# Kernel optimization log

Measured on AMD Instinct MI355X. Metric: run time of the kernel, lower is better.

The kernel has to match this reference:

```python
import jax, jax.numpy as jnp
import numpy as np

NUM_HEADS = 8
BLOCK_SIZE = 32   # tokens per block
WINDOW = 64       # window radius in blocks -> attends to blocks [i-64, i+64]


def setup_inputs() -> dict:
    key = jax.random.key(0)
    ks = jax.random.split(key, 5)
    B, N, C = 8, 8192, 512
    s = 0.02
    return {
        "x": jax.random.normal(ks[0], (B, N, C), dtype=jnp.float32),
        # torch Linear(dim, 3*dim): y = x @ W.T + b; we store W already transposed [in, out]
        "W_qkv": jax.random.normal(ks[1], (C, 3 * C), dtype=jnp.float32) * s,
        "b_qkv": jax.random.normal(ks[2], (3 * C,), dtype=jnp.float32) * s,
        "W_proj": jax.random.normal(ks[3], (C, C), dtype=jnp.float32) * s,
        "b_proj": jax.random.normal(ks[4], (C,), dtype=jnp.float32) * s,
    }


def reference(x, W_qkv, b_qkv, W_proj, b_proj):
    B, N, C = x.shape
    h = NUM_HEADS
    dh = C // h
    scale = jnp.asarray(dh, x.dtype) ** -0.5

    # qkv projection, then the module's head-interleaved split:
    # rearrange 'b n (h d) -> b h n d' with d = 3C/h, chunk(3) on last dim,
    # rearrange back 'b h n d -> b n (h d)'. Equivalent to:
    qkv = (x @ W_qkv + b_qkv).reshape(B, N, h, 3 * dh)
    q = qkv[..., :dh].reshape(B, N, C)
    k = qkv[..., dh:2 * dh].reshape(B, N, C)
    v = qkv[..., 2 * dh:].reshape(B, N, C)

    # dynamic blocking (N chosen divisible by BLOCK_SIZE -> no padding)
    nb = N // BLOCK_SIZE
    qb = q.reshape(B, nb, BLOCK_SIZE, C)
    kb = k.reshape(B, nb, BLOCK_SIZE, C)
    vb = v.reshape(B, nb, BLOCK_SIZE, C)

    # per-offset block attention: query block i, position s attends to
    # position s of every block j in [i-WINDOW, i+WINDOW]
    attn = jnp.einsum('bisc,bjsc->bisj', qb, kb) * scale  # [B, nb, s, nb]
    i_idx = jnp.arange(nb)[:, None]
    j_idx = jnp.arange(nb)[None, :]
    band = (j_idx >= i_idx - WINDOW) & (j_idx <= i_idx + WINDOW)  # [nb, nb]
    neg = jnp.finfo(attn.dtype).min
    attn = jnp.where(band[None, :, None, :], attn, neg)
    attn = jax.nn.softmax(attn, axis=-1)
    out = jnp.einsum('bisj,bjsc->bisc', attn, vb)  # [B, nb, s, C]
    out = out.reshape(B, N, C)

    # 'b n (h d) -> b n h d -> b n (h d)' is the identity
    return out @ W_proj + b_proj
```

## Files before the change

### kernel.cpp

```cpp
#include <hip/hip_runtime.h>
#include <hip/hip_bf16.h>
#include <stdint.h>

#define B_   8
#define N_   8192
#define C_   512
#define NB   256
#define WIN  64

typedef __attribute__((ext_vector_type(8))) short short8;
typedef __attribute__((ext_vector_type(4))) float f32x4;
typedef __hip_bfloat16 bf16;

__device__ __forceinline__ void gload_lds16(const void* g, void* l) {
  __builtin_amdgcn_global_load_lds((const __attribute__((address_space(1))) void*)g,
                                   (__attribute__((address_space(3))) void*)l, 16, 0, 0);
}

__device__ __forceinline__ f32x4 mfma16(short8 a, short8 b, f32x4 c) {
  return __builtin_amdgcn_mfma_f32_16x16x32_bf16(a, b, c, 0, 0, 0);
}


__global__ __launch_bounds__(256) void k_conv_x(const float4* __restrict__ x,
                                                ushort4* __restrict__ xb) {
  size_t idx = (size_t)blockIdx.x * 256 + threadIdx.x;
  float4 v = x[idx];
  union { ushort4 u; bf16 b[4]; } o;
  o.b[0] = __float2bfloat16(v.x); o.b[1] = __float2bfloat16(v.y);
  o.b[2] = __float2bfloat16(v.z); o.b[3] = __float2bfloat16(v.w);
  xb[idx] = o.u;
}

__global__ __launch_bounds__(256) void k_conv_wqkv(const float* __restrict__ W,
                                                   const float* __restrict__ bq,
                                                   bf16* __restrict__ Wt,
                                                   float* __restrict__ bperm) {
  int o = blockIdx.x;
  int part = o >> 9;
  int c = o & 511;
  int h = c >> 6, d = c & 63;
  int src = h * 192 + part * 64 + d;
  for (int kk = threadIdx.x; kk < 512; kk += 256)
    Wt[(size_t)o * 512 + kk] = __float2bfloat16(W[(size_t)kk * 1536 + src]);
  if (threadIdx.x == 0) bperm[o] = bq[src];
}

__global__ __launch_bounds__(256) void k_conv_wproj(const float* __restrict__ W,
                                                    bf16* __restrict__ Wt) {
  int o = blockIdx.x;
  for (int kk = threadIdx.x; kk < 512; kk += 256)
    Wt[(size_t)o * 512 + kk] = __float2bfloat16(W[(size_t)kk * 512 + o]);
}

template <int EPI>
__global__ __launch_bounds__(512, 2) void k_gemm(const bf16* __restrict__ A,
                                                 const bf16* __restrict__ Bt,
                                                 const float* __restrict__ bias,
                                                 bf16* __restrict__ qb,
                                                 bf16* __restrict__ kb,
                                                 bf16* __restrict__ vb,
                                                 float* __restrict__ outf,
                                                 int NT) {
  extern __shared__ bf16 sm[];
  const int tid = threadIdx.x;
  const int lane = tid & 63, wid = tid >> 6;
  const int wr = wid >> 2, wcn = wid & 3;
  const int l15 = lane & 15, l4 = lane >> 4;

  const int nwg = gridDim.x;
  const int cpx = nwg >> 3;
  const int swz = (blockIdx.x & 7) * cpx + (blockIdx.x >> 3);
  const int mt = swz / NT, nt = swz % NT;
  const size_t m0 = (size_t)mt * 256;
  const int n0 = nt * 256;

  f32x4 acc[8][4];
#pragma unroll
  for (int fi = 0; fi < 8; ++fi)
#pragma unroll
    for (int fj = 0; fj < 4; ++fj) acc[fi][fj] = (f32x4){0.f, 0.f, 0.f, 0.f};

#define STAGEG(slot, k0)                                                       \
  {                                                                            \
    bf16* Adst = sm + (slot) * 32768;                                          \
    bf16* Bdst = Adst + 16384;                                                 \
    _Pragma("unroll") for (int i = 0; i < 4; ++i) {                            \
      int li = i * 512 + tid;                                                  \
      int row = li >> 3, ch = li & 7;                                          \
      int chs = ch ^ (row & 7);                                                \
      gload_lds16(A + (m0 + row) * 512 + (k0) + chs * 8,                       \
                  (char*)Adst + li * 16);                                      \
      gload_lds16(Bt + (size_t)(n0 + row) * 512 + (k0) + chs * 8,              \
                  (char*)Bdst + li * 16);                                      \
    }                                                                          \
  }

  STAGEG(0, 0);
  for (int t = 0; t < 8; ++t) {
    if (t < 7) {
      STAGEG((t + 1) & 1, (t + 1) * 64);
      asm volatile("s_waitcnt vmcnt(8)" ::: "memory");
    } else {
      asm volatile("s_waitcnt vmcnt(0)" ::: "memory");
    }
    __builtin_amdgcn_s_barrier();
    __builtin_amdgcn_sched_barrier(0);
    const bf16* Ap = sm + (t & 1) * 32768;
    const bf16* Bp = Ap + 16384;
#pragma unroll
    for (int ks = 0; ks < 2; ++ks) {
      short8 a[8], b[4];
#pragma unroll
      for (int fi = 0; fi < 8; ++fi) {
        int ra = wr * 128 + fi * 16 + l15;
        a[fi] = *(const short8*)&Ap[ra * 64 + (((ks * 4 + l4) ^ (ra & 7)) << 3)];
      }
#pragma unroll
      for (int fj = 0; fj < 4; ++fj) {
        int rb = wcn * 64 + fj * 16 + l15;
        b[fj] = *(const short8*)&Bp[rb * 64 + (((ks * 4 + l4) ^ (rb & 7)) << 3)];
      }
      __builtin_amdgcn_s_setprio(1);
#pragma unroll
      for (int fi = 0; fi < 8; ++fi)
#pragma unroll
        for (int fj = 0; fj < 4; ++fj)
          acc[fi][fj] = mfma16(a[fi], b[fj], acc[fi][fj]);
      __builtin_amdgcn_s_setprio(0);
    }
    __builtin_amdgcn_sched_barrier(0);
    __builtin_amdgcn_s_barrier();
  }
#undef STAGEG

  if (EPI == 0) {
#pragma unroll
    for (int fi = 0; fi < 8; ++fi)
#pragma unroll
      for (int fj = 0; fj < 4; ++fj) {
        int o = n0 + wcn * 64 + fj * 16 + l15;
        float bia = bias[o];
        int part = o >> 9;
        int c = o & 511;
        bf16* dst = part == 0 ? qb : (part == 1 ? kb : vb);
#pragma unroll
        for (int r = 0; r < 4; ++r) {
          size_t m = m0 + wr * 128 + fi * 16 + l4 * 4 + r;
          int bidx = (int)(m >> 13);
          int n = (int)(m & 8191);
          int blk = n >> 5, s = n & 31;
          size_t di = (((size_t)(bidx * 32 + s) * 256 + blk) << 9) | c;
          dst[di] = __float2bfloat16(acc[fi][fj][r] + bia);
        }
      }
  } else {
#pragma unroll
    for (int fi = 0; fi < 8; ++fi)
#pragma unroll
      for (int fj = 0; fj < 4; ++fj) {
        int o = n0 + wcn * 64 + fj * 16 + l15;
        float bia = bias[o];
#pragma unroll
        for (int r = 0; r < 4; ++r) {
          size_t m = m0 + wr * 128 + fi * 16 + l4 * 4 + r;
          outf[m * 512 + o] = acc[fi][fj][r] + bia;
        }
      }
  }
}

__global__ __launch_bounds__(256) void k_transpose_v(const bf16* __restrict__ v,
                                                     bf16* __restrict__ vT) {
  __shared__ bf16 t[32][36];
  int bs = blockIdx.x, j0 = blockIdx.y * 32, c0 = blockIdx.z * 32;
  const bf16* src = v + (size_t)bs * NB * C_;
  bf16* dst = vT + (size_t)bs * C_ * NB;
  int r = threadIdx.x >> 3, c4 = (threadIdx.x & 7) * 4;
  *(ushort4*)&t[r][c4] = *(const ushort4*)(src + (size_t)(j0 + r) * C_ + c0 + c4);
  __syncthreads();
  union { ushort4 u; bf16 b[4]; } o;
  o.b[0] = t[c4 + 0][r]; o.b[1] = t[c4 + 1][r];
  o.b[2] = t[c4 + 2][r]; o.b[3] = t[c4 + 3][r];
  *(ushort4*)(dst + (size_t)(c0 + r) * NB + j0 + c4) = o.u;
}

#define QS_OFF   0
#define KB_OFF   32768
#define VB_OFF   98304
#define SS_OFF   131072
#define PS_OFF   135296
#define SR_OFF   137856
#define MR_OFF   141952
#define LR_OFF   142080
#define AL_OFF   142208
#define ATTN_LDS 142336

__global__ __launch_bounds__(512) void k_attn(const bf16* __restrict__ qg,
                                              const bf16* __restrict__ kg,
                                              const bf16* __restrict__ vTg,
                                              bf16* __restrict__ outb) {
  extern __shared__ char smc[];
  float* Ssf  = (float*)(smc + SS_OFF);
  bf16*  Psb  = (bf16*)(smc + PS_OFF);
  float* Sred = (float*)(smc + SR_OFF);
  float* mrow = (float*)(smc + MR_OFF);
  float* lrow = (float*)(smc + LR_OFF);
  float* alph = (float*)(smc + AL_OFF);

  const int tid = threadIdx.x, lane = tid & 63, wid = tid >> 6;
  const int l15 = lane & 15, l4 = lane >> 4;
  const int gt = (blockIdx.x & 7) * 256 + (blockIdx.x >> 3);
  const int bs = gt >> 3;
  const int b = bs >> 5, s = bs & 31;
  const int i0 = (gt & 7) * 32;
  const int jlo = max(0, i0 - WIN);
  const int jhi = min(NB - 1, i0 + 31 + WIN);
  const int nch = (jhi - jlo + 1) >> 5;
  const bf16* Qb = qg + (size_t)bs * NB * C_;
  const bf16* Kb = kg + (size_t)bs * NB * C_;
  const bf16* Vb = vTg + (size_t)bs * C_ * NB;

  const int qh_qk = (wid >> 2) & 1, jh = (wid >> 1) & 1, ks = wid & 1;
  const int qh_pv = wid >> 2, cq = wid & 3;

  f32x4 O[8];
#pragma unroll
  for (int f = 0; f < 8; ++f) O[f] = (f32x4){0.f, 0.f, 0.f, 0.f};

  if (tid < 32) { mrow[tid] = -1e30f; lrow[tid] = 0.f; }

#pragma unroll
  for (int q = 0; q < 4; ++q) {
    int li = q * 512 + tid;
    int row = li >> 6, g = (li & 63) ^ (row & 15);
    gload_lds16(Qb + (size_t)(i0 + row) * C_ + g * 8, smc + QS_OFF + li * 16);
  }
#pragma unroll
  for (int q = 0; q < 4; ++q) {
    int li = q * 512 + tid;
    int row = li >> 6, g = (li & 63) ^ (row & 15);
    gload_lds16(Kb + (size_t)(jlo + row) * C_ + g * 8, smc + KB_OFF + li * 16);
  }

  for (int t = 0; t < nch; ++t) {
    const int j0 = jlo + t * 32;
    asm volatile("s_waitcnt vmcnt(0) lgkmcnt(0)" ::: "memory");
    __builtin_amdgcn_s_barrier();
    __builtin_amdgcn_sched_barrier(0);

#pragma unroll
    for (int q = 0; q < 4; ++q) {
      int li = q * 512 + tid;
      int c = li >> 2, g = (li & 3) ^ (c & 3);
      gload_lds16(Vb + (size_t)c * NB + j0 + g * 8, smc + VB_OFF + li * 16);
    }
    if (t + 1 < nch) {
      int jn = j0 + 32;
      char* kdst = smc + KB_OFF + ((t + 1) & 1) * 32768;
#pragma unroll
      for (int q = 0; q < 4; ++q) {
        int li = q * 512 + tid;
        int row = li >> 6, g = (li & 63) ^ (row & 15);
        gload_lds16(Kb + (size_t)(jn + row) * C_ + g * 8, kdst + li * 16);
      }
    }

    {
      const int arow = qh_qk * 16 + l15;
      const int brow = jh * 16 + l15;
      const char* Qbase = smc + QS_OFF + arow * 1024;
      const char* Kbase = smc + KB_OFF + (t & 1) * 32768 + brow * 1024;
      f32x4 a0 = (f32x4){0.f, 0.f, 0.f, 0.f}, a1 = a0;
      __builtin_amdgcn_s_setprio(1);
#pragma unroll
      for (int cc = 0; cc < 8; ++cc) {
        int sa = (ks * 32 + cc * 4 + l4) ^ (arow & 15);
        int sb = (ks * 32 + cc * 4 + l4) ^ (brow & 15);
        short8 av = *(const short8*)(Qbase + sa * 16);
        short8 bv = *(const short8*)(Kbase + sb * 16);
        if (cc & 1) a1 = mfma16(av, bv, a1);
        else        a0 = mfma16(av, bv, a0);
      }
      __builtin_amdgcn_s_setprio(0);
      f32x4 acc = a0 + a1;
      if (ks) {
        *(f32x4*)&Sred[(wid >> 1) * 256 + lane * 4] = acc;
      }
      asm volatile("s_waitcnt lgkmcnt(0)" ::: "memory");
      __builtin_amdgcn_s_barrier();
      __builtin_amdgcn_sched_barrier(0);
      if (!ks) {
        f32x4 su = acc + *(f32x4*)&Sred[(wid >> 1) * 256 + lane * 4];
        int jg = j0 + jh * 16 + l15;
#pragma unroll
        for (int r = 0; r < 4; ++r) {
          int i_in = qh_qk * 16 + l4 * 4 + r;
          int i_abs = i0 + i_in;
          bool valid = (jg >= i_abs - WIN) && (jg <= i_abs + WIN);
          Ssf[i_in * 33 + jh * 16 + l15] = valid ? su[r] * 0.125f : -1e30f;
        }
      }
      asm volatile("s_waitcnt lgkmcnt(0)" ::: "memory");
      __builtin_amdgcn_s_barrier();
      __builtin_amdgcn_sched_barrier(0);
    }

    {
      int row = tid >> 4, u = tid & 15;
      float s0 = Ssf[row * 33 + u], s1 = Ssf[row * 33 + u + 16];
      float mc = fmaxf(s0, s1);
      mc = fmaxf(mc, __shfl_xor(mc, 1));
      mc = fmaxf(mc, __shfl_xor(mc, 2));
      mc = fmaxf(mc, __shfl_xor(mc, 4));
      mc = fmaxf(mc, __shfl_xor(mc, 8));
      float mo = mrow[row];
      float mn = fmaxf(mo, mc);
      float a = __expf(mo - mn);
      float p0 = __expf(s0 - mn), p1 = __expf(s1 - mn);
      float ps = p0 + p1;
      ps += __shfl_xor(ps, 1);
      ps += __shfl_xor(ps, 2);
      ps += __shfl_xor(ps, 4);
      ps += __shfl_xor(ps, 8);
      if (u == 0) {
        lrow[row] = lrow[row] * a + ps;
        mrow[row] = mn;
        alph[row] = a;
      }
      Psb[row * 40 + u] = __float2bfloat16(p0);
      Psb[row * 40 + u + 16] = __float2bfloat16(p1);
    }
    if (t + 1 < nch)
      asm volatile("s_waitcnt vmcnt(4) lgkmcnt(0)" ::: "memory");
    else
      asm volatile("s_waitcnt vmcnt(0) lgkmcnt(0)" ::: "memory");
    __builtin_amdgcn_s_barrier();
    __builtin_amdgcn_sched_barrier(0);

    {
      float ar[4];
#pragma unroll
      for (int r = 0; r < 4; ++r) ar[r] = alph[qh_pv * 16 + l4 * 4 + r];
      short8 pa = *(const short8*)(smc + PS_OFF + (qh_pv * 16 + l15) * 80 + l4 * 16);
      __builtin_amdgcn_s_setprio(1);
#pragma unroll
      for (int f = 0; f < 8; ++f) {
        int c = cq * 128 + f * 16 + l15;
        short8 vv = *(const short8*)(smc + VB_OFF + c * 64 + ((l4 ^ (c & 3)) << 4));
#pragma unroll
        for (int r = 0; r < 4; ++r) O[f][r] *= ar[r];
        O[f] = mfma16(pa, vv, O[f]);
      }
      __builtin_amdgcn_s_setprio(0);
    }
    __builtin_amdgcn_sched_barrier(0);
  }

  asm volatile("s_waitcnt lgkmcnt(0)" ::: "memory");
  __builtin_amdgcn_s_barrier();
  {
    float lr[4];
#pragma unroll
    for (int r = 0; r < 4; ++r) lr[r] = 1.f / lrow[qh_pv * 16 + l4 * 4 + r];
#pragma unroll
    for (int f = 0; f < 8; ++f) {
      int c = cq * 128 + f * 16 + l15;
#pragma unroll
      for (int r = 0; r < 4; ++r) {
        int il = qh_pv * 16 + l4 * 4 + r;
        int n = (i0 + il) * 32 + s;
        outb[((size_t)b * N_ + n) * C_ + c] = __float2bfloat16(O[f][r] * lr[r]);
      }
    }
  }
}

extern "C" void kernel_launch(void* const* d_in, const int* in_sizes, int n_in,
                              void* d_out, int out_size, void* d_ws, size_t ws_size,
                              hipStream_t stream) {
  const float* x = (const float*)d_in[0];
  const float* Wqkv = (const float*)d_in[1];
  const float* bqkv = (const float*)d_in[2];
  const float* Wproj = (const float*)d_in[3];
  const float* bproj = (const float*)d_in[4];

  char* ws = (char*)d_ws;
  const size_t SLOT = 67108864ull;
  bf16* slotA = (bf16*)ws;
  bf16* slotB = (bf16*)(ws + SLOT);
  bf16* Wqkv_t = (bf16*)(ws + 2 * SLOT);
  bf16* Wproj_t = (bf16*)(ws + 2 * SLOT + 1572864);
  float* bias_perm = (float*)(ws + 2 * SLOT + 1572864 + 524288);
  bf16* qbuf = (bf16*)d_out;
  bf16* kbuf = qbuf + 33554432ull;

  static int attr_done = 0;
  if (!attr_done) {
    hipFuncSetAttribute((const void*)k_gemm<0>,
                        hipFuncAttributeMaxDynamicSharedMemorySize, 131072);
    hipFuncSetAttribute((const void*)k_gemm<1>,
                        hipFuncAttributeMaxDynamicSharedMemorySize, 131072);
    hipFuncSetAttribute((const void*)k_attn,
                        hipFuncAttributeMaxDynamicSharedMemorySize, ATTN_LDS);
    attr_done = 1;
  }

  k_conv_x<<<32768, 256, 0, stream>>>((const float4*)x, (ushort4*)slotA);
  k_conv_wqkv<<<1536, 256, 0, stream>>>(Wqkv, bqkv, Wqkv_t, bias_perm);
  k_conv_wproj<<<512, 256, 0, stream>>>(Wproj, Wproj_t);

  k_gemm<0><<<256 * 6, 512, 131072, stream>>>(slotA, Wqkv_t, bias_perm,
                                              qbuf, kbuf, slotB, nullptr, 6);
  k_transpose_v<<<dim3(256, 8, 16), 256, 0, stream>>>(slotB, slotA);
  k_attn<<<2048, 512, ATTN_LDS, stream>>>(qbuf, kbuf, slotA, slotB);
  k_gemm<1><<<256 * 2, 512, 131072, stream>>>(slotB, Wproj_t, bproj,
                                              nullptr, nullptr, nullptr, (float*)d_out, 2);
}
```

Before: 339.1 us.

## Fuse V transpose into QKV GEMM epilogue, tile weight conversion, restructure GEMM loop

The QKV GEMM epilogue now writes V directly in transposed [bs, c, blk] layout, which removes the separate transpose kernel and its extra pass over V. Weight conversion kernels are merged into one LDS-tiled transpose kernel, so global reads are coalesced. The GEMM main loop changes its warp-to-fragment mapping (interleaved rows and columns), loads all fragments for a 64-wide K slice up front, and waits on vmcnt(0) at the end of each iteration instead of vmcnt(8). The transposed V stores are 2-byte scattered writes with a 512-byte stride, which may cost more than the removed transpose kernel did.

```diff
diff --git a/kernel.cpp b/kernel.cpp
--- a/kernel.cpp
+++ b/kernel.cpp
@@ -32,25 +32,30 @@
   xb[idx] = o.u;
 }
 
-__global__ __launch_bounds__(256) void k_conv_wqkv(const float* __restrict__ W,
-                                                   const float* __restrict__ bq,
-                                                   bf16* __restrict__ Wt,
-                                                   float* __restrict__ bperm) {
-  int o = blockIdx.x;
-  int part = o >> 9;
-  int c = o & 511;
-  int h = c >> 6, d = c & 63;
-  int src = h * 192 + part * 64 + d;
-  for (int kk = threadIdx.x; kk < 512; kk += 256)
-    Wt[(size_t)o * 512 + kk] = __float2bfloat16(W[(size_t)kk * 1536 + src]);
-  if (threadIdx.x == 0) bperm[o] = bq[src];
-}
-
-__global__ __launch_bounds__(256) void k_conv_wproj(const float* __restrict__ W,
-                                                    bf16* __restrict__ Wt) {
-  int o = blockIdx.x;
-  for (int kk = threadIdx.x; kk < 512; kk += 256)
-    Wt[(size_t)o * 512 + kk] = __float2bfloat16(W[(size_t)kk * 512 + o]);
+__global__ __launch_bounds__(256) void k_conv_w(const float* __restrict__ W,
+                                                const float* __restrict__ bsrc,
+                                                bf16* __restrict__ Wt,
+                                                float* __restrict__ bperm,
+                                                int ldw, int qkv) {
+  __shared__ float tile[32][65];
+  const int cc = blockIdx.x, k0 = blockIdx.y * 32;
+  const int src0 = cc * 64;
+  const int o0 = qkv ? ((cc % 3) * 512 + (cc / 3) * 64) : src0;
+  const int tid = threadIdx.x;
+#pragma unroll
+  for (int q = 0; q < 8; ++q) {
+    int li = q * 256 + tid;
+    int r = li >> 6, c = li & 63;
+    tile[r][c] = W[(size_t)(k0 + r) * ldw + src0 + c];
+  }
+  __syncthreads();
+#pragma unroll
+  for (int q = 0; q < 8; ++q) {
+    int li = q * 256 + tid;
+    int c2 = li >> 5, kk = li & 31;
+    Wt[(size_t)(o0 + c2) * 512 + k0 + kk] = __float2bfloat16(tile[kk][c2]);
+  }
+  if (qkv && blockIdx.y == 0 && tid < 64) bperm[o0 + tid] = bsrc[src0 + tid];
 }
 
 template <int EPI>
@@ -62,7 +67,7 @@
                                                  bf16* __restrict__ vb,
                                                  float* __restrict__ outf,
                                                  int NT) {
-  extern __shared__ bf16 sm[];
+  extern __shared__ char gsm[];
   const int tid = threadIdx.x;
   const int lane = tid & 63, wid = tid >> 6;
   const int wr = wid >> 2, wcn = wid & 3;
@@ -81,77 +86,105 @@
 #pragma unroll
     for (int fj = 0; fj < 4; ++fj) acc[fi][fj] = (f32x4){0.f, 0.f, 0.f, 0.f};
 
-#define STAGEG(slot, k0)                                                       \
+#define STAGE(E, K0)                                                           \
   {                                                                            \
-    bf16* Adst = sm + (slot) * 32768;                                          \
-    bf16* Bdst = Adst + 16384;                                                 \
-    _Pragma("unroll") for (int i = 0; i < 4; ++i) {                            \
-      int li = i * 512 + tid;                                                  \
-      int row = li >> 3, ch = li & 7;                                          \
-      int chs = ch ^ (row & 7);                                                \
-      gload_lds16(A + (m0 + row) * 512 + (k0) + chs * 8,                       \
-                  (char*)Adst + li * 16);                                      \
-      gload_lds16(Bt + (size_t)(n0 + row) * 512 + (k0) + chs * 8,              \
-                  (char*)Bdst + li * 16);                                      \
+    _Pragma("unroll") for (int q = 0; q < 4; ++q) {                            \
+      int li = q * 512 + tid;                                                  \
+      int r = li >> 3, g = (li & 7) ^ (r & 7);                                 \
+      gload_lds16(A + (m0 + r) * 512 + (K0) + g * 8,                           \
+                  gsm + (E) * 65536 + li * 16);                                \
     }                                                                          \
-  }
-
-  STAGEG(0, 0);
+    _Pragma("unroll") for (int q = 0; q < 4; ++q) {                            \
+      int li = q * 512 + tid;                                                  \
+      int r = li >> 3, g = (li & 7) ^ (r & 7);                                 \
+      gload_lds16(Bt + (size_t)(n0 + r) * 512 + (K0) + g * 8,                  \
+                  gsm + (E) * 65536 + 32768 + li * 16);                        \
+    }                                                                          \
+  }
+
+  STAGE(0, 0);
+  asm volatile("s_waitcnt vmcnt(0)" ::: "memory");
+  __builtin_amdgcn_s_barrier();
+  __builtin_amdgcn_sched_barrier(0);
+
   for (int t = 0; t < 8; ++t) {
-    if (t < 7) {
-      STAGEG((t + 1) & 1, (t + 1) * 64);
-      asm volatile("s_waitcnt vmcnt(8)" ::: "memory");
-    } else {
-      asm volatile("s_waitcnt vmcnt(0)" ::: "memory");
-    }
+    const int d = t & 1;
+    if (t < 7) STAGE(d ^ 1, (t + 1) * 64);
+    __builtin_amdgcn_sched_barrier(0);
+    const char* Ab = gsm + d * 65536;
+    const char* Bb = Ab + 32768;
+
+    short8 a0[4][2], a1[4][2], bfr[4][2];
+#pragma unroll
+    for (int f = 0; f < 4; ++f) {
+      int ra = f * 32 + wr * 16 + l15;
+      const char* base = Ab + ra * 128;
+      a0[f][0] = *(const short8*)(base + ((l4 ^ (ra & 7)) << 4));
+      a0[f][1] = *(const short8*)(base + (((4 + l4) ^ (ra & 7)) << 4));
+    }
+#pragma unroll
+    for (int f = 0; f < 4; ++f) {
+      int rb = f * 64 + wcn * 16 + l15;
+      const char* base = Bb + rb * 128;
+      bfr[f][0] = *(const short8*)(base + ((l4 ^ (rb & 7)) << 4));
+      bfr[f][1] = *(const short8*)(base + (((4 + l4) ^ (rb & 7)) << 4));
+    }
+#pragma unroll
+    for (int f = 0; f < 4; ++f) {
+      int ra = 128 + f * 32 + wr * 16 + l15;
+      const char* base = Ab + ra * 128;
+      a1[f][0] = *(const short8*)(base + ((l4 ^ (ra & 7)) << 4));
+      a1[f][1] = *(const short8*)(base + (((4 + l4) ^ (ra & 7)) << 4));
+    }
+
+    __builtin_amdgcn_s_setprio(1);
+#pragma unroll
+    for (int f = 0; f < 4; ++f)
+#pragma unroll
+      for (int g = 0; g < 4; ++g) {
+        acc[f][g] = mfma16(a0[f][0], bfr[g][0], acc[f][g]);
+        acc[f][g] = mfma16(a0[f][1], bfr[g][1], acc[f][g]);
+      }
+#pragma unroll
+    for (int f = 0; f < 4; ++f)
+#pragma unroll
+      for (int g = 0; g < 4; ++g) {
+        acc[4 + f][g] = mfma16(a1[f][0], bfr[g][0], acc[4 + f][g]);
+        acc[4 + f][g] = mfma16(a1[f][1], bfr[g][1], acc[4 + f][g]);
+      }
+    __builtin_amdgcn_s_setprio(0);
+
+    __builtin_amdgcn_sched_barrier(0);
+    asm volatile("s_waitcnt vmcnt(0)" ::: "memory");
     __builtin_amdgcn_s_barrier();
     __builtin_amdgcn_sched_barrier(0);
-    const bf16* Ap = sm + (t & 1) * 32768;
-    const bf16* Bp = Ap + 16384;
-#pragma unroll
-    for (int ks = 0; ks < 2; ++ks) {
-      short8 a[8], b[4];
-#pragma unroll
-      for (int fi = 0; fi < 8; ++fi) {
-        int ra = wr * 128 + fi * 16 + l15;
-        a[fi] = *(const short8*)&Ap[ra * 64 + (((ks * 4 + l4) ^ (ra & 7)) << 3)];
-      }
+  }
+#undef STAGE
+
+  if (EPI == 0) {
+#pragma unroll
+    for (int fi = 0; fi < 8; ++fi)
 #pragma unroll
       for (int fj = 0; fj < 4; ++fj) {
-        int rb = wcn * 64 + fj * 16 + l15;
-        b[fj] = *(const short8*)&Bp[rb * 64 + (((ks * 4 + l4) ^ (rb & 7)) << 3)];
-      }
-      __builtin_amdgcn_s_setprio(1);
-#pragma unroll
-      for (int fi = 0; fi < 8; ++fi)
-#pragma unroll
-        for (int fj = 0; fj < 4; ++fj)
-          acc[fi][fj] = mfma16(a[fi], b[fj], acc[fi][fj]);
-      __builtin_amdgcn_s_setprio(0);
-    }
-    __builtin_amdgcn_sched_barrier(0);
-    __builtin_amdgcn_s_barrier();
-  }
-#undef STAGEG
-
-  if (EPI == 0) {
-#pragma unroll
-    for (int fi = 0; fi < 8; ++fi)
-#pragma unroll
-      for (int fj = 0; fj < 4; ++fj) {
-        int o = n0 + wcn * 64 + fj * 16 + l15;
+        int o = n0 + fj * 64 + wcn * 16 + l15;
         float bia = bias[o];
         int part = o >> 9;
         int c = o & 511;
-        bf16* dst = part == 0 ? qb : (part == 1 ? kb : vb);
 #pragma unroll
         for (int r = 0; r < 4; ++r) {
-          size_t m = m0 + wr * 128 + fi * 16 + l4 * 4 + r;
+          size_t m = m0 + fi * 32 + wr * 16 + l4 * 4 + r;
           int bidx = (int)(m >> 13);
           int n = (int)(m & 8191);
           int blk = n >> 5, s = n & 31;
-          size_t di = (((size_t)(bidx * 32 + s) * 256 + blk) << 9) | c;
-          dst[di] = __float2bfloat16(acc[fi][fj][r] + bia);
+          int bs = bidx * 32 + s;
+          bf16 val = __float2bfloat16(acc[fi][fj][r] + bia);
+          if (part == 0) {
+            qb[(((size_t)bs * 256 + blk) << 9) | c] = val;
+          } else if (part == 1) {
+            kb[(((size_t)bs * 256 + blk) << 9) | c] = val;
+          } else {
+            vb[((size_t)bs * 512 + c) * 256 + blk] = val;
+          }
         }
       }
   } else {
@@ -159,30 +192,15 @@
     for (int fi = 0; fi < 8; ++fi)
 #pragma unroll
       for (int fj = 0; fj < 4; ++fj) {
-        int o = n0 + wcn * 64 + fj * 16 + l15;
+        int o = n0 + fj * 64 + wcn * 16 + l15;
         float bia = bias[o];
 #pragma unroll
         for (int r = 0; r < 4; ++r) {
-          size_t m = m0 + wr * 128 + fi * 16 + l4 * 4 + r;
+          size_t m = m0 + fi * 32 + wr * 16 + l4 * 4 + r;
           outf[m * 512 + o] = acc[fi][fj][r] + bia;
         }
       }
   }
-}
-
-__global__ __launch_bounds__(256) void k_transpose_v(const bf16* __restrict__ v,
-                                                     bf16* __restrict__ vT) {
-  __shared__ bf16 t[32][36];
-  int bs = blockIdx.x, j0 = blockIdx.y * 32, c0 = blockIdx.z * 32;
-  const bf16* src = v + (size_t)bs * NB * C_;
-  bf16* dst = vT + (size_t)bs * C_ * NB;
-  int r = threadIdx.x >> 3, c4 = (threadIdx.x & 7) * 4;
-  *(ushort4*)&t[r][c4] = *(const ushort4*)(src + (size_t)(j0 + r) * C_ + c0 + c4);
-  __syncthreads();
-  union { ushort4 u; bf16 b[4]; } o;
-  o.b[0] = t[c4 + 0][r]; o.b[1] = t[c4 + 1][r];
-  o.b[2] = t[c4 + 2][r]; o.b[3] = t[c4 + 3][r];
-  *(ushort4*)(dst + (size_t)(c0 + r) * NB + j0 + c4) = o.u;
 }
 
 #define QS_OFF   0
@@ -407,13 +425,12 @@
   }
 
   k_conv_x<<<32768, 256, 0, stream>>>((const float4*)x, (ushort4*)slotA);
-  k_conv_wqkv<<<1536, 256, 0, stream>>>(Wqkv, bqkv, Wqkv_t, bias_perm);
-  k_conv_wproj<<<512, 256, 0, stream>>>(Wproj, Wproj_t);
-
-  k_gemm<0><<<256 * 6, 512, 131072, stream>>>(slotA, Wqkv_t, bias_perm,
-                                              qbuf, kbuf, slotB, nullptr, 6);
-  k_transpose_v<<<dim3(256, 8, 16), 256, 0, stream>>>(slotB, slotA);
-  k_attn<<<2048, 512, ATTN_LDS, stream>>>(qbuf, kbuf, slotA, slotB);
-  k_gemm<1><<<256 * 2, 512, 131072, stream>>>(slotB, Wproj_t, bproj,
-                                              nullptr, nullptr, nullptr, (float*)d_out, 2);
-}
+  k_conv_w<<<dim3(24, 16), 256, 0, stream>>>(Wqkv, bqkv, Wqkv_t, bias_perm, 1536, 1);
+  k_conv_w<<<dim3(8, 16), 256, 0, stream>>>(Wproj, nullptr, Wproj_t, nullptr, 512, 0);
+
+  k_gemm<0><<<1536, 512, 131072, stream>>>(slotA, Wqkv_t, bias_perm,
+                                           qbuf, kbuf, slotB, nullptr, 6);
+  k_attn<<<2048, 512, ATTN_LDS, stream>>>(qbuf, kbuf, slotB, slotA);
+  k_gemm<1><<<512, 512, 131072, stream>>>(slotA, Wproj_t, bproj,
+                                          nullptr, nullptr, nullptr, (float*)d_out, 2);
+}
```

Result: slower. 546.9 us (+61.3%).
